# Kernel tuning notes

Measured on AMD Instinct MI355X. Metric: run time of the kernel, lower is better.

## Reference

```python
import jax, jax.numpy as jnp
import numpy as np
from jax import lax

D_MODEL = 512; D_FF = 2048
D_STATE = 16; D_CONV = 4; EXPAND = 2          # mamba_ssm defaults
D_INNER = EXPAND * D_MODEL                    # 1024
DT_RANK = (D_MODEL + 15) // 16                # 32
B, W, C, D = 2, 1024, 64, 8                   # C*D == D_MODEL


def setup_inputs():
    key = jax.random.key(0)
    ks = jax.random.split(key, 24)
    def p(k, shape, s=0.02):
        return jax.random.normal(k, shape, jnp.float32) * s
    inp = {"x": jax.random.normal(ks[0], (B, W, C, D), jnp.float32)}
    for i, pref in enumerate(["fm", "bm"]):
        o = 1 + i * 7
        inp[pref + "_in_W"] = p(ks[o], (2 * D_INNER, D_MODEL))
        inp[pref + "_conv_W"] = p(ks[o + 1], (D_INNER, D_CONV))
        inp[pref + "_conv_b"] = jnp.zeros((D_INNER,), jnp.float32)
        inp[pref + "_xproj_W"] = p(ks[o + 2], (DT_RANK + 2 * D_STATE, D_INNER))
        inp[pref + "_dt_W"] = p(ks[o + 3], (D_INNER, DT_RANK))
        inp[pref + "_dt_b"] = p(ks[o + 4], (D_INNER,), 0.1)
        inp[pref + "_A_log"] = jnp.log(jnp.broadcast_to(
            jnp.arange(1, D_STATE + 1, dtype=jnp.float32), (D_INNER, D_STATE)))
        inp[pref + "_D"] = jnp.ones((D_INNER,), jnp.float32)
        inp[pref + "_out_W"] = p(ks[o + 5], (D_MODEL, D_INNER))
    inp["ln1_g"] = jnp.ones((D_MODEL,), jnp.float32); inp["ln1_b"] = jnp.zeros((D_MODEL,), jnp.float32)
    inp["ln2_g"] = jnp.ones((D_MODEL,), jnp.float32); inp["ln2_b"] = jnp.zeros((D_MODEL,), jnp.float32)
    inp["ln3_g"] = jnp.ones((D_MODEL,), jnp.float32); inp["ln3_b"] = jnp.zeros((D_MODEL,), jnp.float32)
    inp["ff_W1"] = p(ks[15], (D_FF, D_MODEL)); inp["ff_b1"] = jnp.zeros((D_FF,), jnp.float32)
    inp["ff_W2"] = p(ks[16], (D_MODEL, D_FF)); inp["ff_b2"] = jnp.zeros((D_MODEL,), jnp.float32)
    return inp


def _silu(x):
    return x * jax.nn.sigmoid(x)


def _layernorm(x, g, b, eps=1e-5):
    mu = jnp.mean(x, -1, keepdims=True)
    var = jnp.var(x, -1, keepdims=True)
    return (x - mu) * lax.rsqrt(var + eps) * g + b


def _mamba(u, in_W, conv_W, conv_b, xproj_W, dt_W, dt_b, A_log, Dp, out_W):
    # u: (B, L, d_model). Standard Mamba block (mamba_ssm reference math).
    xz = jnp.einsum('bld,ed->ble', u, in_W)            # (B, L, 2*d_inner)
    xm, z = jnp.split(xz, 2, axis=-1)
    # causal depthwise conv along L
    xc = lax.conv_general_dilated(
        xm.transpose(0, 2, 1), conv_W[:, None, :], (1,),
        [(D_CONV - 1, 0)], feature_group_count=D_INNER)
    xm = _silu((xc + conv_b[None, :, None]).transpose(0, 2, 1))  # (B, L, d_inner)
    dbc = jnp.einsum('bld,ed->ble', xm, xproj_W)       # (B, L, dt_rank + 2*d_state)
    dt = dbc[..., :DT_RANK]
    Bm = dbc[..., DT_RANK:DT_RANK + D_STATE]           # (B, L, d_state)
    Cm = dbc[..., DT_RANK + D_STATE:]                  # (B, L, d_state)
    delta = jax.nn.softplus(jnp.einsum('blr,dr->bld', dt, dt_W) + dt_b)  # (B, L, d_inner)
    A = -jnp.exp(A_log)                                # (d_inner, d_state)
    dA = jnp.exp(delta[..., None] * A)                 # (B, L, d_inner, d_state)
    dBu = delta[..., None] * Bm[:, :, None, :] * xm[..., None]

    def step(h, inputs):
        dA_t, dBu_t = inputs
        h = dA_t * h + dBu_t
        return h, h

    h0 = jnp.zeros((u.shape[0], D_INNER, D_STATE), u.dtype)
    _, hs = lax.scan(step, h0, (dA.transpose(1, 0, 2, 3), dBu.transpose(1, 0, 2, 3)))
    y = jnp.einsum('lbds,lbs->bld', hs, Cm.transpose(1, 0, 2))
    y = y + xm * Dp
    y = y * _silu(z)
    return jnp.einsum('ble,de->bld', y, out_W)         # (B, L, d_model)


def reference(x,
              fm_in_W, fm_conv_W, fm_conv_b, fm_xproj_W, fm_dt_W, fm_dt_b, fm_A_log, fm_D, fm_out_W,
              bm_in_W, bm_conv_W, bm_conv_b, bm_xproj_W, bm_dt_W, bm_dt_b, bm_A_log, bm_D, bm_out_W,
              ln1_g, ln1_b, ln2_g, ln2_b, ln3_g, ln3_b,
              ff_W1, ff_b1, ff_W2, ff_b2):
    b, w, c, d = x.shape
    xf = x.reshape(b, w, c * d)
    fwd = _mamba(xf, fm_in_W, fm_conv_W, fm_conv_b, fm_xproj_W, fm_dt_W, fm_dt_b, fm_A_log, fm_D, fm_out_W)
    bwd = jnp.flip(_mamba(jnp.flip(xf, 1), bm_in_W, bm_conv_W, bm_conv_b, bm_xproj_W,
                          bm_dt_W, bm_dt_b, bm_A_log, bm_D, bm_out_W), 1)
    an1 = _layernorm(xf + fwd, ln1_g, ln1_b)   # AddNorm: LN(x + dropout(y)); dropout off at eval
    an2 = _layernorm(xf + bwd, ln2_g, ln2_b)
    out = an1 + an2
    h = jnp.maximum(jnp.einsum('bld,fd->blf', out, ff_W1) + ff_b1, 0)
    ff = jnp.einsum('blf,df->bld', h, ff_W2) + ff_b2
    out = _layernorm(ff + ff, ln3_g, ln3_b)    # an3(out, out) == LN(out + out)
    return out.reshape(b, w, c, d)
```

## Files before the change

kernel.cpp:

```cpp
#include <hip/hip_runtime.h>
#include <hip/hip_bf16.h>
#include <math.h>

#define MM 2048
#define BATCH 2
#define SEQ 1024
#define DMODEL 512
#define DINNER 1024
#define DSTATE 16
#define DTRANK 32
#define DFF 2048

#define NCHUNK 16
#define CHUNK 64
#define GTOT 65536

typedef short bf16x8 __attribute__((ext_vector_type(8)));
typedef float floatx4 __attribute__((ext_vector_type(4)));
typedef unsigned short ushort8v __attribute__((ext_vector_type(8)));
typedef unsigned short ushort4v __attribute__((ext_vector_type(4)));

__device__ __forceinline__ unsigned short f2bf(float f) {
    union { float f; unsigned u; } v; v.f = f;
    unsigned r = v.u + 0x7FFF + ((v.u >> 16) & 1);
    return (unsigned short)(r >> 16);
}
__device__ __forceinline__ float bf2f(unsigned short u) {
    union { unsigned u; float f; } v; v.u = ((unsigned)u) << 16; return v.f;
}

__device__ __forceinline__ float quadsum4(float x) {
    union { float f; int i; } a, b;
    a.f = x;
    b.i = __builtin_amdgcn_update_dpp(0, a.i, 0xB1, 0xF, 0xF, false); a.f += b.f;
    b.i = __builtin_amdgcn_update_dpp(0, a.i, 0x4E, 0xF, 0xF, false); a.f += b.f;
    return a.f;
}

#define GLOAD_LDS16(gp, lp) __builtin_amdgcn_global_load_lds( \
    (const __attribute__((address_space(1))) unsigned int*)(gp), \
    (__attribute__((address_space(3))) unsigned int*)(lp), 16, 0, 0)


template<int EPI, int OUTBF16>
__global__ __launch_bounds__(256) void gemm_mfma_batch(
    int M, int N, int K,
    const unsigned short* __restrict__ A0, const unsigned short* __restrict__ A1, int lda,
    const unsigned short* __restrict__ B0, const unsigned short* __restrict__ B1, int ldb,
    const float* __restrict__ bias,
    void* __restrict__ C0, void* __restrict__ C1, int ldc)
{
    __shared__ unsigned short As[2][128 * 32];
    __shared__ unsigned short Bs[2][128 * 32];
    const int z = blockIdx.z;
    const unsigned short* A = z ? A1 : A0;
    const unsigned short* B = z ? B1 : B0;
    void* Cout = z ? C1 : C0;
    const int tid  = threadIdx.x;
    const int wave = tid >> 6;
    const int lane = tid & 63;
    const int bm = blockIdx.y * 128;
    const int bn = blockIdx.x * 128;

    const int strow = lane & 15;
    const int stkc  = lane >> 4;
    const int wr = wave >> 1, wc = wave & 1;
    const int frow = lane & 15;
    const int fkc  = lane >> 4;

    floatx4 acc[4][4];
    #pragma unroll
    for (int i = 0; i < 4; ++i)
        #pragma unroll
        for (int j = 0; j < 4; ++j)
            acc[i][j] = (floatx4){0.f, 0.f, 0.f, 0.f};

    for (int k0 = 0; k0 < K; k0 += 64) {
        __syncthreads();
        #pragma unroll
        for (int hh = 0; hh < 2; ++hh) {
            #pragma unroll
            for (int q = 0; q < 2; ++q) {
                int g = wave * 2 + q;
                GLOAD_LDS16(A + (size_t)(bm + g * 16 + strow) * lda + k0 + hh * 32 + stkc * 8,
                            As[hh] + g * 512);
            }
            #pragma unroll
            for (int q = 0; q < 2; ++q) {
                int g = wave * 2 + q;
                GLOAD_LDS16(B + (size_t)(bn + g * 16 + strow) * ldb + k0 + hh * 32 + stkc * 8,
                            Bs[hh] + g * 512);
            }
        }
        __syncthreads();

        #pragma unroll
        for (int hh = 0; hh < 2; ++hh) {
            bf16x8 af[4], bfr[4];
            #pragma unroll
            for (int i = 0; i < 4; ++i)
                af[i] = *(const bf16x8*)(As[hh] + (wr * 4 + i) * 512 + fkc * 128 + frow * 8);
            #pragma unroll
            for (int j = 0; j < 4; ++j)
                bfr[j] = *(const bf16x8*)(Bs[hh] + (wc * 4 + j) * 512 + fkc * 128 + frow * 8);
            #pragma unroll
            for (int i = 0; i < 4; ++i)
                #pragma unroll
                for (int j = 0; j < 4; ++j)
                    acc[i][j] = __builtin_amdgcn_mfma_f32_16x16x32_bf16(
                        af[i], bfr[j], acc[i][j], 0, 0, 0);
        }
    }

    const int orow0 = bm + wr * 64 + (lane >> 4) * 4;
    const int ocol0 = bn + wc * 64 + (lane & 15);
    #pragma unroll
    for (int j = 0; j < 4; ++j) {
        const int col = ocol0 + j * 16;
        const float bv = bias ? bias[col] : 0.f;
        #pragma unroll
        for (int i = 0; i < 4; ++i) {
            #pragma unroll
            for (int r = 0; r < 4; ++r) {
                int row = orow0 + i * 16 + r;
                float t = acc[i][j][r] + bv;
                if (EPI == 1) t = fmaxf(t, 0.f);
                if (OUTBF16)
                    ((unsigned short*)Cout)[(size_t)row * ldc + col] = f2bf(t);
                else
                    ((float*)Cout)[(size_t)row * ldc + col] = t;
            }
        }
    }
}

__global__ __launch_bounds__(256) void gemm_inproj_kernel(
    const unsigned short* __restrict__ A,
    const unsigned short* __restrict__ B0, const unsigned short* __restrict__ B1,
    unsigned short* __restrict__ Cx0, unsigned short* __restrict__ Cz0,
    unsigned short* __restrict__ Cx1, unsigned short* __restrict__ Cz1)
{
    __shared__ unsigned short As[2][128 * 32];
    __shared__ unsigned short Bs[2][128 * 32];
    const int z = blockIdx.z;
    const unsigned short* B = z ? B1 : B0;
    const int tid  = threadIdx.x;
    const int wave = tid >> 6;
    const int lane = tid & 63;
    const int bm = blockIdx.y * 128;
    const int bn = blockIdx.x * 128;

    const int strow = lane & 15;
    const int stkc  = lane >> 4;
    const int wr = wave >> 1, wc = wave & 1;
    const int frow = lane & 15;
    const int fkc  = lane >> 4;

    floatx4 acc[4][4];
    #pragma unroll
    for (int i = 0; i < 4; ++i)
        #pragma unroll
        for (int j = 0; j < 4; ++j)
            acc[i][j] = (floatx4){0.f, 0.f, 0.f, 0.f};

    for (int k0 = 0; k0 < DMODEL; k0 += 64) {
        __syncthreads();
        #pragma unroll
        for (int hh = 0; hh < 2; ++hh) {
            #pragma unroll
            for (int q = 0; q < 2; ++q) {
                int g = wave * 2 + q;
                GLOAD_LDS16(A + (size_t)(bm + g * 16 + strow) * DMODEL + k0 + hh * 32 + stkc * 8,
                            As[hh] + g * 512);
            }
            #pragma unroll
            for (int q = 0; q < 2; ++q) {
                int g = wave * 2 + q;
                GLOAD_LDS16(B + (size_t)(bn + g * 16 + strow) * DMODEL + k0 + hh * 32 + stkc * 8,
                            Bs[hh] + g * 512);
            }
        }
        __syncthreads();

        #pragma unroll
        for (int hh = 0; hh < 2; ++hh) {
            bf16x8 af[4], bfr[4];
            #pragma unroll
            for (int i = 0; i < 4; ++i)
                af[i] = *(const bf16x8*)(As[hh] + (wr * 4 + i) * 512 + fkc * 128 + frow * 8);
            #pragma unroll
            for (int j = 0; j < 4; ++j)
                bfr[j] = *(const bf16x8*)(Bs[hh] + (wc * 4 + j) * 512 + fkc * 128 + frow * 8);
            #pragma unroll
            for (int i = 0; i < 4; ++i)
                #pragma unroll
                for (int j = 0; j < 4; ++j)
                    acc[i][j] = __builtin_amdgcn_mfma_f32_16x16x32_bf16(
                        af[i], bfr[j], acc[i][j], 0, 0, 0);
        }
    }

    const int zh = bn >= DINNER;
    unsigned short* C = z ? (zh ? Cz1 : Cx1) : (zh ? Cz0 : Cx0);
    const int cb = zh ? DINNER : 0;
    const int orow0 = bm + wr * 64 + (lane >> 4) * 4;
    const int ocol0 = bn + wc * 64 + (lane & 15) - cb;
    #pragma unroll
    for (int j = 0; j < 4; ++j) {
        const int col = ocol0 + j * 16;
        #pragma unroll
        for (int i = 0; i < 4; ++i)
            #pragma unroll
            for (int r = 0; r < 4; ++r)
                C[(size_t)(orow0 + i * 16 + r) * DINNER + col] = f2bf(acc[i][j][r]);
    }
}

template<int NSPLIT>
__global__ __launch_bounds__(256) void gemm_mfma_splitk(
    int M, int N, int K,
    const unsigned short* __restrict__ A0, const unsigned short* __restrict__ A1, int lda,
    const unsigned short* __restrict__ B0, const unsigned short* __restrict__ B1, int ldb,
    float* __restrict__ part, int ldc)
{
    __shared__ unsigned short As[2][128 * 32];
    __shared__ unsigned short Bs[2][128 * 32];
    const int z = blockIdx.z;
    const int dir = z / NSPLIT, sp = z % NSPLIT;
    const unsigned short* A = dir ? A1 : A0;
    const unsigned short* B = dir ? B1 : B0;
    float* Cp = part + (size_t)z * M * ldc;
    const int kbeg = sp * (K / NSPLIT);
    const int kend = kbeg + (K / NSPLIT);
    const int tid  = threadIdx.x;
    const int wave = tid >> 6;
    const int lane = tid & 63;
    const int bm = blockIdx.y * 128;
    const int bn = blockIdx.x * 128;

    const int strow = lane & 15;
    const int stkc  = lane >> 4;
    const int wr = wave >> 1, wc = wave & 1;
    const int frow = lane & 15;
    const int fkc  = lane >> 4;

    floatx4 acc[4][4];
    #pragma unroll
    for (int i = 0; i < 4; ++i)
        #pragma unroll
        for (int j = 0; j < 4; ++j)
            acc[i][j] = (floatx4){0.f, 0.f, 0.f, 0.f};

    for (int k0 = kbeg; k0 < kend; k0 += 64) {
        __syncthreads();
        #pragma unroll
        for (int hh = 0; hh < 2; ++hh) {
            #pragma unroll
            for (int q = 0; q < 2; ++q) {
                int g = wave * 2 + q;
                GLOAD_LDS16(A + (size_t)(bm + g * 16 + strow) * lda + k0 + hh * 32 + stkc * 8,
                            As[hh] + g * 512);
            }
            #pragma unroll
            for (int q = 0; q < 2; ++q) {
                int g = wave * 2 + q;
                GLOAD_LDS16(B + (size_t)(bn + g * 16 + strow) * ldb + k0 + hh * 32 + stkc * 8,
                            Bs[hh] + g * 512);
            }
        }
        __syncthreads();

        #pragma unroll
        for (int hh = 0; hh < 2; ++hh) {
            bf16x8 af[4], bfr[4];
            #pragma unroll
            for (int i = 0; i < 4; ++i)
                af[i] = *(const bf16x8*)(As[hh] + (wr * 4 + i) * 512 + fkc * 128 + frow * 8);
            #pragma unroll
            for (int j = 0; j < 4; ++j)
                bfr[j] = *(const bf16x8*)(Bs[hh] + (wc * 4 + j) * 512 + fkc * 128 + frow * 8);
            #pragma unroll
            for (int i = 0; i < 4; ++i)
                #pragma unroll
                for (int j = 0; j < 4; ++j)
                    acc[i][j] = __builtin_amdgcn_mfma_f32_16x16x32_bf16(
                        af[i], bfr[j], acc[i][j], 0, 0, 0);
        }
    }

    const int orow0 = bm + wr * 64 + (lane >> 4) * 4;
    const int ocol0 = bn + wc * 64 + (lane & 15);
    #pragma unroll
    for (int j = 0; j < 4; ++j) {
        const int col = ocol0 + j * 16;
        #pragma unroll
        for (int i = 0; i < 4; ++i)
            #pragma unroll
            for (int r = 0; r < 4; ++r)
                Cp[(size_t)(orow0 + i * 16 + r) * ldc + col] = acc[i][j][r];
    }
}

__global__ __launch_bounds__(256) void xproj_splitk_kernel(
    const unsigned short* __restrict__ A_f, const unsigned short* __restrict__ A_b,
    const unsigned short* __restrict__ Wf,  const unsigned short* __restrict__ Wb,
    float* __restrict__ part)
{
    __shared__ unsigned short As[2][128 * 32];
    __shared__ unsigned short Bs[2][64 * 32];
    const int tid = threadIdx.x, wave = tid >> 6, lane = tid & 63;
    const int bm = blockIdx.x * 128;
    const int dir = blockIdx.y >> 2, sp = blockIdx.y & 3;
    const unsigned short* A = dir ? A_b : A_f;
    const unsigned short* W = dir ? Wb  : Wf;
    float* Cp = part + (size_t)blockIdx.y * MM * 64;
    const int kbeg = sp * 256, kend = kbeg + 256;

    const int strow = lane & 15;
    const int stkc  = lane >> 4;
    const int frow = lane & 15;
    const int fkc  = lane >> 4;

    floatx4 acc[2][4];
    #pragma unroll
    for (int i = 0; i < 2; ++i)
        #pragma unroll
        for (int j = 0; j < 4; ++j)
            acc[i][j] = (floatx4){0.f, 0.f, 0.f, 0.f};

    for (int k0 = kbeg; k0 < kend; k0 += 64) {
        __syncthreads();
        #pragma unroll
        for (int hh = 0; hh < 2; ++hh) {
            #pragma unroll
            for (int q = 0; q < 2; ++q) {
                int g = wave * 2 + q;
                GLOAD_LDS16(A + (size_t)(bm + g * 16 + strow) * DINNER + k0 + hh * 32 + stkc * 8,
                            As[hh] + g * 512);
            }
            GLOAD_LDS16(W + (size_t)(wave * 16 + strow) * DINNER + k0 + hh * 32 + stkc * 8,
                        Bs[hh] + wave * 512);
        }
        __syncthreads();

        #pragma unroll
        for (int hh = 0; hh < 2; ++hh) {
            bf16x8 af[2], bfr[4];
            #pragma unroll
            for (int i = 0; i < 2; ++i)
                af[i] = *(const bf16x8*)(As[hh] + (wave * 2 + i) * 512 + fkc * 128 + frow * 8);
            #pragma unroll
            for (int j = 0; j < 4; ++j)
                bfr[j] = *(const bf16x8*)(Bs[hh] + j * 512 + fkc * 128 + frow * 8);
            #pragma unroll
            for (int i = 0; i < 2; ++i)
                #pragma unroll
                for (int j = 0; j < 4; ++j)
                    acc[i][j] = __builtin_amdgcn_mfma_f32_16x16x32_bf16(
                        af[i], bfr[j], acc[i][j], 0, 0, 0);
        }
    }

    const int orow0 = bm + wave * 32 + (lane >> 4) * 4;
    #pragma unroll
    for (int j = 0; j < 4; ++j) {
        const int col = (lane & 15) + j * 16;
        #pragma unroll
        for (int i = 0; i < 2; ++i)
            #pragma unroll
            for (int r = 0; r < 4; ++r)
                Cp[(size_t)(orow0 + i * 16 + r) * 64 + col] = acc[i][j][r];
    }
}

__global__ __launch_bounds__(256) void xproj_reduce_kernel(
    const float* __restrict__ part,
    float* __restrict__ dbc_f, float* __restrict__ dbc_b,
    float* __restrict__ bct_f, float* __restrict__ bct_b)
{
    const int dir = blockIdx.y;
    const int i = (blockIdx.x * 256 + threadIdx.x) * 4;
    const float* p = part + (size_t)dir * 4 * (MM * 64);
    float4 a = *(const float4*)(p + i);
    #pragma unroll
    for (int s = 1; s < 4; ++s) {
        float4 t = *(const float4*)(p + (size_t)s * (MM * 64) + i);
        a.x += t.x; a.y += t.y; a.z += t.z; a.w += t.w;
    }
    const int m = i >> 6, c = i & 63;
    if (c < 32) {
        float* dbc = dir ? dbc_b : dbc_f;
        *(float4*)(dbc + (size_t)m * 32 + c) = a;
    } else {
        float* bct = dir ? bct_b : bct_f;
        *(float4*)(bct + (size_t)m * 32 + (c - 32)) = a;
    }
}

__global__ __launch_bounds__(256) void dtproj_batch_kernel(
    int M, int N, int K,
    const float* __restrict__ A0, const float* __restrict__ A1, int lda,
    const float* __restrict__ B0, const float* __restrict__ B1, int ldb,
    const float* __restrict__ bias0, const float* __restrict__ bias1,
    unsigned short* __restrict__ C0, unsigned short* __restrict__ C1, int ldc)
{
    __shared__ float As[16][64];
    __shared__ float Bs[16][64];
    const int z = blockIdx.z;
    const float* A = z ? A1 : A0;
    const float* B = z ? B1 : B0;
    const float* biasR = z ? bias1 : bias0;
    unsigned short* C = z ? C1 : C0;
    const int tid = threadIdx.x;
    const int tx = tid & 15, ty = tid >> 4;
    const int bm = blockIdx.y * 64, bn = blockIdx.x * 64;
    const int lm = tid & 63;
    const int lk = (tid >> 6) * 4;
    const float* Arow = A + (size_t)(bm + lm) * lda + lk;
    const float* Brow = B + (size_t)(bn + lm) * ldb + lk;
    float acc[4][4] = {};
    for (int k0 = 0; k0 < K; k0 += 16) {
        float4 av = *(const float4*)(Arow + k0);
        float4 bv = *(const float4*)(Brow + k0);
        __syncthreads();
        As[lk+0][lm] = av.x; As[lk+1][lm] = av.y; As[lk+2][lm] = av.z; As[lk+3][lm] = av.w;
        Bs[lk+0][lm] = bv.x; Bs[lk+1][lm] = bv.y; Bs[lk+2][lm] = bv.z; Bs[lk+3][lm] = bv.w;
        __syncthreads();
        #pragma unroll
        for (int k = 0; k < 16; ++k) {
            float4 a = *(const float4*)(&As[k][ty*4]);
            float4 b = *(const float4*)(&Bs[k][tx*4]);
            float ar[4] = {a.x,a.y,a.z,a.w};
            float br[4] = {b.x,b.y,b.z,b.w};
            #pragma unroll
            for (int i = 0; i < 4; ++i)
                #pragma unroll
                for (int j = 0; j < 4; ++j)
                    acc[i][j] = fmaf(ar[i], br[j], acc[i][j]);
        }
    }
    const int row0 = bm + ty*4, col0 = bn + tx*4;
    #pragma unroll
    for (int i = 0; i < 4; ++i) {
        float br = biasR[row0 + i];
        ushort4v o;
        #pragma unroll
        for (int j = 0; j < 4; ++j) {
            float t = acc[i][j] + br;
            o[j] = f2bf(fmaxf(t, 0.f) + log1pf(__expf(-fabsf(t))));
        }
        *(ushort4v*)(C + (size_t)(row0 + i) * ldc + col0) = o;
    }
}

__global__ __launch_bounds__(256) void cast_pre_kernel(
    const float* __restrict__ x, const float* __restrict__ w0,
    const float* __restrict__ w1, const float* __restrict__ xp0,
    const float* __restrict__ xp1, unsigned short* __restrict__ dst)
{
    int i = (blockIdx.x * 256 + threadIdx.x) * 8;
    const float* src; int off;
    if      (i < 1048576) { src = x;   off = 0; }
    else if (i < 2097152) { src = w0;  off = 1048576; }
    else if (i < 3145728) { src = w1;  off = 2097152; }
    else if (i < 3211264) { src = xp0; off = 3145728; }
    else                  { src = xp1; off = 3211264; }
    float4 a = *(const float4*)(src + i - off);
    float4 b = *(const float4*)(src + i - off + 4);
    ushort8v o;
    o[0] = f2bf(a.x); o[1] = f2bf(a.y); o[2] = f2bf(a.z); o[3] = f2bf(a.w);
    o[4] = f2bf(b.x); o[5] = f2bf(b.y); o[6] = f2bf(b.z); o[7] = f2bf(b.w);
    *(ushort8v*)(dst + i) = o;
}

__global__ __launch_bounds__(256) void cast_post_kernel(
    const float* __restrict__ w0, const float* __restrict__ w1,
    const float* __restrict__ w2, const float* __restrict__ w3,
    unsigned short* __restrict__ dst)
{
    int i = (blockIdx.x * 256 + threadIdx.x) * 8;
    const float* src; int off;
    if      (i < 524288)  { src = w0; off = 0; }
    else if (i < 1048576) { src = w1; off = 524288; }
    else if (i < 2097152) { src = w2; off = 1048576; }
    else                  { src = w3; off = 2097152; }
    float4 a = *(const float4*)(src + i - off);
    float4 b = *(const float4*)(src + i - off + 4);
    ushort8v o;
    o[0] = f2bf(a.x); o[1] = f2bf(a.y); o[2] = f2bf(a.z); o[3] = f2bf(a.w);
    o[4] = f2bf(b.x); o[5] = f2bf(b.y); o[6] = f2bf(b.z); o[7] = f2bf(b.w);
    *(ushort8v*)(dst + i) = o;
}

__global__ __launch_bounds__(256) void conv_silu_tr_kernel(
    const unsigned short* __restrict__ x_f, const unsigned short* __restrict__ x_b,
    const float* __restrict__ Wf,  const float* __restrict__ Wb,
    const float* __restrict__ cbf, const float* __restrict__ cbb,
    unsigned short* __restrict__ of,  unsigned short* __restrict__ ob,
    unsigned short* __restrict__ otf, unsigned short* __restrict__ otb)
{
    __shared__ unsigned short t[32][34];
    const int dir = blockIdx.z;
    const unsigned short* xo = dir ? x_b : x_f;
    const float* convW = dir ? Wb : Wf;
    const float* convb = dir ? cbb : cbf;
    unsigned short* xm  = dir ? ob : of;
    unsigned short* xmT = dir ? otb : otf;
    const int m0 = blockIdx.x * 32, d0 = blockIdx.y * 32;
    const int tx = threadIdx.x & 31, ty = threadIdx.x >> 5;
    const int d = d0 + tx;
    float4 wv = *(const float4*)(convW + d * 4);
    float w[4] = {wv.x, wv.y, wv.z, wv.w};
    const float cb = convb[d];
    #pragma unroll
    for (int rr = 0; rr < 32; rr += 8) {
        int m = m0 + ty + rr;
        int b = m >> 10, l = m & (SEQ - 1);
        float acc = cb;
        #pragma unroll
        for (int j = 0; j < 4; ++j) {
            int p = dir ? (l + 3 - j) : (l - 3 + j);
            if (p >= 0 && p < SEQ)
                acc = fmaf(bf2f(xo[(size_t)(b * SEQ + p) * DINNER + d]), w[j], acc);
        }
        float sig = 1.f / (1.f + __expf(-acc));
        unsigned short v = f2bf(acc * sig);
        xm[(size_t)m * DINNER + d] = v;
        t[ty + rr][tx] = v;
    }
    __syncthreads();
    #pragma unroll
    for (int rr = 0; rr < 32; rr += 8)
        xmT[(size_t)(d0 + ty + rr) * MM + m0 + tx] = t[tx][ty + rr];
}

template<int DIR>
__device__ __forceinline__ void pass1_body(
    const unsigned short* __restrict__ deltaT, const unsigned short* __restrict__ xmT,
    const float* __restrict__ bct, const float* __restrict__ Alog,
    const float* __restrict__ Dv,
    unsigned short* __restrict__ y0T, float* __restrict__ cumT,
    float* __restrict__ Pout, float* __restrict__ Hout)
{
    const int tid = threadIdx.x;
    const int sq = tid & 3;
    const int dloc = tid >> 2;
    const int d = blockIdx.x * 64 + dloc;
    const int b = blockIdx.y / NCHUNK;
    const int c = blockIdx.y % NCHUNK;

    float4 Av = *(const float4*)(Alog + d * DSTATE + sq * 4);
    const float A0 = -__expf(Av.x), A1 = -__expf(Av.y);
    const float A2 = -__expf(Av.z), A3 = -__expf(Av.w);
    const float Dp = Dv[d];
    const unsigned short* dRow = deltaT + (size_t)d * MM + b * SEQ;
    const unsigned short* xRow = xmT + (size_t)d * MM + b * SEQ;
    const float* bcRow = bct + (size_t)(b * SEQ) * 32 + sq * 4;
    unsigned short* yRow = y0T + (size_t)d * MM + b * SEQ;
    float* uRow = cumT + (size_t)d * MM + b * SEQ;

    float h0 = 0.f, h1 = 0.f, h2 = 0.f, h3 = 0.f, sdl = 0.f;
    const int segBase = DIR ? (SEQ - CHUNK - c * CHUNK) : (c * CHUNK);
    for (int ii = 0; ii < CHUNK; ii += 8) {
        const int off = DIR ? (segBase + (CHUNK - 8) - ii) : (segBase + ii);
        ushort8v dl8 = *(const ushort8v*)(dRow + off);
        ushort8v x8  = *(const ushort8v*)(xRow + off);
        float yv[8], cu[8];
        #pragma unroll
        for (int u = 0; u < 8; ++u) {
            const int t = DIR ? (7 - u) : u;
            float4 Bv = *(const float4*)(bcRow + (size_t)(off + t) * 32);
            float4 Cv = *(const float4*)(bcRow + (size_t)(off + t) * 32 + 16);
            float dlv = bf2f(dl8[t]);
            float xv  = bf2f(x8[t]);
            sdl += dlv;
            float dx = dlv * xv;
            h0 = fmaf(__expf(dlv * A0), h0, dx * Bv.x);
            h1 = fmaf(__expf(dlv * A1), h1, dx * Bv.y);
            h2 = fmaf(__expf(dlv * A2), h2, dx * Bv.z);
            h3 = fmaf(__expf(dlv * A3), h3, dx * Bv.w);
            float part = h0 * Cv.x + h1 * Cv.y + h2 * Cv.z + h3 * Cv.w;
            part = quadsum4(part);
            yv[t] = fmaf(xv, Dp, part);
            cu[t] = sdl;
        }
        if (sq == 0) {
            ushort8v y8;
            #pragma unroll
            for (int u = 0; u < 8; ++u) y8[u] = f2bf(yv[u]);
            *(ushort8v*)(yRow + off) = y8;
            *(float4*)(uRow + off)     = (float4){cu[0], cu[1], cu[2], cu[3]};
            *(float4*)(uRow + off + 4) = (float4){cu[4], cu[5], cu[6], cu[7]};
        }
    }
    const size_t g4 = ((size_t)(DIR * BATCH + b) * DINNER + d) * DSTATE + sq * 4;
    *(float4*)(Pout + (size_t)c * GTOT + g4) =
        (float4){__expf(sdl * A0), __expf(sdl * A1), __expf(sdl * A2), __expf(sdl * A3)};
    *(float4*)(Hout + (size_t)c * GTOT + g4) = (float4){h0, h1, h2, h3};
}

__global__ __launch_bounds__(256) void scan_pass1_kernel(
    const unsigned short* __restrict__ dT_f, const unsigned short* __restrict__ dT_b,
    const unsigned short* __restrict__ xT_f, const unsigned short* __restrict__ xT_b,
    const float* __restrict__ bct_f, const float* __restrict__ bct_b,
    const float* __restrict__ Alog_f, const float* __restrict__ Alog_b,
    const float* __restrict__ D_f, const float* __restrict__ D_b,
    unsigned short* __restrict__ y0T_f, unsigned short* __restrict__ y0T_b,
    float* __restrict__ cumT_f, float* __restrict__ cumT_b,
    float* __restrict__ Pout, float* __restrict__ Hout)
{
    if (blockIdx.z == 0)
        pass1_body<0>(dT_f, xT_f, bct_f, Alog_f, D_f, y0T_f, cumT_f, Pout, Hout);
    else
        pass1_body<1>(dT_b, xT_b, bct_b, Alog_b, D_b, y0T_b, cumT_b, Pout, Hout);
}

__global__ __launch_bounds__(256) void scan_carry_kernel(
    const float* __restrict__ P, const float* __restrict__ H,
    float* __restrict__ carry)
{
    const int g = blockIdx.x * 256 + threadIdx.x;
    float p[NCHUNK], hh[NCHUNK];
    #pragma unroll
    for (int c = 0; c < NCHUNK; ++c) {
        p[c]  = P[(size_t)c * GTOT + g];
        hh[c] = H[(size_t)c * GTOT + g];
    }
    float h = 0.f;
    #pragma unroll
    for (int c = 0; c < NCHUNK; ++c) {
        carry[(size_t)c * GTOT + g] = h;
        h = fmaf(p[c], h, hh[c]);
    }
}

__global__ __launch_bounds__(256) void scan_correct_kernel(
    const unsigned short* __restrict__ y0T_f, const unsigned short* __restrict__ y0T_b,
    const float* __restrict__ cumT_f, const float* __restrict__ cumT_b,
    const float* __restrict__ bct_f, const float* __restrict__ bct_b,
    const float* __restrict__ Alog_f, const float* __restrict__ Alog_b,
    const float* __restrict__ carry,
    const unsigned short* __restrict__ z_f, const unsigned short* __restrict__ z_b,
    unsigned short* __restrict__ ybf_f, unsigned short* __restrict__ ybf_b)
{
    __shared__ float Cs[16][33];
    __shared__ float Asm[32][16];
    __shared__ float Cy[32][16];
    __shared__ float t[32][33];

    const int dir = blockIdx.z;
    const unsigned short* y0T = dir ? y0T_b : y0T_f;
    const float* cumT = dir ? cumT_b : cumT_f;
    const float* bct  = dir ? bct_b  : bct_f;
    const float* Alog = dir ? Alog_b : Alog_f;
    const unsigned short* zon = dir ? z_b : z_f;
    unsigned short* ybf = dir ? ybf_b : ybf_f;

    const int m0 = blockIdx.x * 32, d0 = blockIdx.y * 32;
    const int b = m0 >> 10;
    const int l0 = m0 & (SEQ - 1);
    const int c = dir ? ((SEQ - 1 - l0) >> 6) : (l0 >> 6);

    for (int idx = threadIdx.x; idx < 512; idx += 256) {
        int s1 = idx & 15, ml = idx >> 4;
        Cs[s1][ml] = bct[(size_t)(m0 + ml) * 32 + 16 + s1];
        int dl2 = idx >> 4, s2 = idx & 15;
        Asm[dl2][s2] = -__expf(Alog[(d0 + dl2) * DSTATE + s2]);
        Cy[dl2][s2] = carry[(size_t)c * GTOT
            + ((size_t)(dir * BATCH + b) * DINNER + d0 + dl2) * DSTATE + s2];
    }
    __syncthreads();

    const int tx = threadIdx.x & 31, ty = threadIdx.x >> 5;
    #pragma unroll
    for (int rr = 0; rr < 32; rr += 8) {
        const int dloc = ty + rr;
        const size_t base = (size_t)(d0 + dloc) * MM + m0 + tx;
        float u  = cumT[base];
        float y0 = bf2f(y0T[base]);
        float corr = 0.f;
        #pragma unroll
        for (int s = 0; s < DSTATE; ++s)
            corr = fmaf(Cs[s][tx] * Cy[dloc][s], __expf(Asm[dloc][s] * u), corr);
        t[dloc][tx] = y0 + corr;
    }
    __syncthreads();
    #pragma unroll
    for (int rr = 0; rr < 32; rr += 8) {
        int m = m0 + ty + rr, d = d0 + tx;
        float z = bf2f(zon[(size_t)m * DINNER + d]);
        float sig = 1.f / (1.f + __expf(-z));
        ybf[(size_t)m * DINNER + d] = f2bf(t[tx][ty + rr] * (z * sig));
    }
}

__global__ __launch_bounds__(256) void reduce_ff1_kernel(
    const float* __restrict__ part, const float* __restrict__ bias,
    unsigned short* __restrict__ outh)
{
    const int i = (blockIdx.x * 256 + threadIdx.x) * 4;
    float4 a = *(const float4*)(part + i);
    float4 b = *(const float4*)(part + (size_t)MM * DFF + i);
    const int c = i & (DFF - 1);
    ushort4v o;
    o[0] = f2bf(fmaxf(a.x + b.x + bias[c],     0.f));
    o[1] = f2bf(fmaxf(a.y + b.y + bias[c + 1], 0.f));
    o[2] = f2bf(fmaxf(a.z + b.z + bias[c + 2], 0.f));
    o[3] = f2bf(fmaxf(a.w + b.w + bias[c + 3], 0.f));
    *(ushort4v*)(outh + i) = o;
}

__global__ __launch_bounds__(256) void ln_combine_fused_kernel(
    const float* __restrict__ xf, const float* __restrict__ part,
    const float* __restrict__ g1, const float* __restrict__ b1,
    const float* __restrict__ g2, const float* __restrict__ b2,
    unsigned short* __restrict__ out)
{
    const int m = blockIdx.x;
    const int tid = threadIdx.x;
    const size_t stride = (size_t)MM * DMODEL;
    const float* xr = xf + (size_t)m * DMODEL;
    const float* p = part + (size_t)m * DMODEL;
    float v1a = xr[tid], v1b = xr[tid + 256];
    float v2a = xr[tid], v2b = xr[tid + 256];
    #pragma unroll
    for (int k = 0; k < 4; ++k) {
        v1a += p[k * stride + tid];       v1b += p[k * stride + tid + 256];
        v2a += p[(4 + k) * stride + tid]; v2b += p[(4 + k) * stride + tid + 256];
    }
    float s1 = v1a + v1b, q1 = v1a*v1a + v1b*v1b;
    float s2 = v2a + v2b, q2 = v2a*v2a + v2b*v2b;
    #pragma unroll
    for (int off = 32; off; off >>= 1) {
        s1 += __shfl_xor(s1, off); q1 += __shfl_xor(q1, off);
        s2 += __shfl_xor(s2, off); q2 += __shfl_xor(q2, off);
    }
    __shared__ float sm[4][4];
    const int w = tid >> 6;
    if ((tid & 63) == 0) { sm[w][0] = s1; sm[w][1] = q1; sm[w][2] = s2; sm[w][3] = q2; }
    __syncthreads();
    s1 = sm[0][0] + sm[1][0] + sm[2][0] + sm[3][0];
    q1 = sm[0][1] + sm[1][1] + sm[2][1] + sm[3][1];
    s2 = sm[0][2] + sm[1][2] + sm[2][2] + sm[3][2];
    q2 = sm[0][3] + sm[1][3] + sm[2][3] + sm[3][3];
    const float inv = 1.f / DMODEL;
    float mu1 = s1 * inv, mu2 = s2 * inv;
    float rs1 = rsqrtf(q1 * inv - mu1 * mu1 + 1e-5f);
    float rs2 = rsqrtf(q2 * inv - mu2 * mu2 + 1e-5f);
    unsigned short* orow = out + (size_t)m * DMODEL;
    orow[tid]       = f2bf((v1a - mu1) * rs1 * g1[tid]       + b1[tid]
                         + (v2a - mu2) * rs2 * g2[tid]       + b2[tid]);
    orow[tid + 256] = f2bf((v1b - mu1) * rs1 * g1[tid + 256] + b1[tid + 256]
                         + (v2b - mu2) * rs2 * g2[tid + 256] + b2[tid + 256]);
}

__global__ __launch_bounds__(256) void ln_final_fused_kernel(
    const float* __restrict__ part, const float* __restrict__ bias,
    const float* __restrict__ g, const float* __restrict__ b,
    float* __restrict__ out)
{
    const int m = blockIdx.x;
    const int tid = threadIdx.x;
    const size_t stride = (size_t)MM * DMODEL;
    const float* p = part + (size_t)m * DMODEL;
    float fa = bias[tid], fb = bias[tid + 256];
    #pragma unroll
    for (int k = 0; k < 8; ++k) {
        fa += p[k * stride + tid];
        fb += p[k * stride + tid + 256];
    }
    float va = 2.f * fa, vb = 2.f * fb;
    float s = va + vb, q = va*va + vb*vb;
    #pragma unroll
    for (int off = 32; off; off >>= 1) {
        s += __shfl_xor(s, off); q += __shfl_xor(q, off);
    }
    __shared__ float sm[4][2];
    const int w = tid >> 6;
    if ((tid & 63) == 0) { sm[w][0] = s; sm[w][1] = q; }
    __syncthreads();
    s = sm[0][0] + sm[1][0] + sm[2][0] + sm[3][0];
    q = sm[0][1] + sm[1][1] + sm[2][1] + sm[3][1];
    const float inv = 1.f / DMODEL;
    float mu = s * inv;
    float rs = rsqrtf(q * inv - mu * mu + 1e-5f);
    float* orow = out + (size_t)m * DMODEL;
    orow[tid]       = (va - mu) * rs * g[tid]       + b[tid];
    orow[tid + 256] = (vb - mu) * rs * g[tid + 256] + b[tid + 256];
}

extern "C" void kernel_launch(void* const* d_in, const int* in_sizes, int n_in,
                              void* d_out, int out_size, void* d_ws, size_t ws_size,
                              hipStream_t stream)
{
    const float* x         = (const float*)d_in[0];
    const float* fm_in_W   = (const float*)d_in[1];
    const float* fm_conv_W = (const float*)d_in[2];
    const float* fm_conv_b = (const float*)d_in[3];
    const float* fm_xproj_W= (const float*)d_in[4];
    const float* fm_dt_W   = (const float*)d_in[5];
    const float* fm_dt_b   = (const float*)d_in[6];
    const float* fm_A_log  = (const float*)d_in[7];
    const float* fm_D      = (const float*)d_in[8];
    const float* fm_out_W  = (const float*)d_in[9];
    const float* bm_in_W   = (const float*)d_in[10];
    const float* bm_conv_W = (const float*)d_in[11];
    const float* bm_conv_b = (const float*)d_in[12];
    const float* bm_xproj_W= (const float*)d_in[13];
    const float* bm_dt_W   = (const float*)d_in[14];
    const float* bm_dt_b   = (const float*)d_in[15];
    const float* bm_A_log  = (const float*)d_in[16];
    const float* bm_D      = (const float*)d_in[17];
    const float* bm_out_W  = (const float*)d_in[18];
    const float* ln1_g     = (const float*)d_in[19];
    const float* ln1_b     = (const float*)d_in[20];
    const float* ln2_g     = (const float*)d_in[21];
    const float* ln2_b     = (const float*)d_in[22];
    const float* ln3_g     = (const float*)d_in[23];
    const float* ln3_b     = (const float*)d_in[24];
    const float* ff_W1     = (const float*)d_in[25];
    const float* ff_b1     = (const float*)d_in[26];
    const float* ff_W2     = (const float*)d_in[27];
    const float* ff_b2     = (const float*)d_in[28];
    float* out = (float*)d_out;

    float* ws = (float*)d_ws;
    size_t o = 0;
    unsigned short* xbf_f = (unsigned short*)(ws + o); o += (size_t)MM * DINNER / 2;
    unsigned short* xbf_b = (unsigned short*)(ws + o); o += (size_t)MM * DINNER / 2;
    unsigned short* zbf_f = (unsigned short*)(ws + o); o += (size_t)MM * DINNER / 2;
    unsigned short* zbf_b = (unsigned short*)(ws + o); o += (size_t)MM * DINNER / 2;
    unsigned short* xm_bf_f = (unsigned short*)(ws + o); o += (size_t)MM * DINNER / 2;
    unsigned short* xm_bf_b = (unsigned short*)(ws + o); o += (size_t)MM * DINNER / 2;
    unsigned short* xmT_f   = (unsigned short*)(ws + o); o += (size_t)MM * DINNER / 2;
    unsigned short* xmT_b   = (unsigned short*)(ws + o); o += (size_t)MM * DINNER / 2;
    unsigned short* deltaT_f= (unsigned short*)(ws + o); o += (size_t)MM * DINNER / 2;
    unsigned short* deltaT_b= (unsigned short*)(ws + o); o += (size_t)MM * DINNER / 2;
    float* dbc_f    = ws + o; o += (size_t)MM * 32;
    float* dbc_b    = ws + o; o += (size_t)MM * 32;
    float* bct_f    = ws + o; o += (size_t)MM * 32;
    float* bct_b    = ws + o; o += (size_t)MM * 32;
    unsigned short* y0T_f = (unsigned short*)(ws + o); o += (size_t)MM * DINNER / 2;
    unsigned short* y0T_b = (unsigned short*)(ws + o); o += (size_t)MM * DINNER / 2;
    float* scanP    = ws + o; o += (size_t)NCHUNK * (GTOT / 16) * 16;
    float* scanH    = ws + o; o += (size_t)NCHUNK * (GTOT / 16) * 16;
    float* scanCy   = ws + o; o += (size_t)NCHUNK * (GTOT / 16) * 16;
    float* gpart    = ws + o; o += (size_t)8 * MM * DMODEL;

    float* cumT_f = gpart;
    float* cumT_b = gpart + (size_t)MM * DINNER;
    unsigned short* xin_bf     = (unsigned short*)scanP;
    unsigned short* fm_inW_bf  = xin_bf + 1048576;
    unsigned short* bm_inW_bf  = fm_inW_bf + 1048576;
    unsigned short* fm_xpW_bf  = bm_inW_bf + 1048576;
    unsigned short* bm_xpW_bf  = fm_xpW_bf + 65536;
    unsigned short* ybf_f = (unsigned short*)scanP;
    unsigned short* ybf_b = (unsigned short*)scanH;
    unsigned short* fm_outW_bf = (unsigned short*)zbf_f;
    unsigned short* bm_outW_bf = fm_outW_bf + 524288;
    unsigned short* W1_bf      = bm_outW_bf + 524288;
    unsigned short* W2_bf      = W1_bf + 1048576;
    unsigned short* outsum_bf  = (unsigned short*)xbf_f;
    unsigned short* h_bf = (unsigned short*)deltaT_f;

    cast_pre_kernel<<<3276800 / 2048, 256, 0, stream>>>(
        x, fm_in_W, bm_in_W, fm_xproj_W, bm_xproj_W, xin_bf);

    gemm_inproj_kernel<<<dim3(2048/128, MM/128, 2), 256, 0, stream>>>(
        xin_bf, fm_inW_bf, bm_inW_bf, xbf_f, zbf_f, xbf_b, zbf_b);

    conv_silu_tr_kernel<<<dim3(MM/32, DINNER/32, 2), 256, 0, stream>>>(
        xbf_f, xbf_b, fm_conv_W, bm_conv_W, fm_conv_b, bm_conv_b,
        xm_bf_f, xm_bf_b, xmT_f, xmT_b);

    xproj_splitk_kernel<<<dim3(MM/128, 8), 256, 0, stream>>>(
        xm_bf_f, xm_bf_b, fm_xpW_bf, bm_xpW_bf, gpart);
    xproj_reduce_kernel<<<dim3((MM*64)/1024, 2), 256, 0, stream>>>(
        gpart, dbc_f, dbc_b, bct_f, bct_b);

    dtproj_batch_kernel<<<dim3(MM/64, DINNER/64, 2), 256, 0, stream>>>(
        DINNER, MM, DTRANK, fm_dt_W, bm_dt_W, DTRANK, dbc_f, dbc_b, 32,
        fm_dt_b, bm_dt_b, deltaT_f, deltaT_b, MM);

    scan_pass1_kernel<<<dim3(DINNER/64, BATCH*NCHUNK, 2), 256, 0, stream>>>(
        deltaT_f, deltaT_b, xmT_f, xmT_b, bct_f, bct_b,
        fm_A_log, bm_A_log, fm_D, bm_D,
        y0T_f, y0T_b, cumT_f, cumT_b, scanP, scanH);
    scan_carry_kernel<<<GTOT/256, 256, 0, stream>>>(scanP, scanH, scanCy);
    scan_correct_kernel<<<dim3(MM/32, DINNER/32, 2), 256, 0, stream>>>(
        y0T_f, y0T_b, cumT_f, cumT_b, bct_f, bct_b, fm_A_log, bm_A_log,
        scanCy, zbf_f, zbf_b, ybf_f, ybf_b);

    cast_post_kernel<<<3145728 / 2048, 256, 0, stream>>>(
        fm_out_W, bm_out_W, ff_W1, ff_W2, fm_outW_bf);

    gemm_mfma_splitk<4><<<dim3(DMODEL/128, MM/128, 8), 256, 0, stream>>>(
        MM, DMODEL, DINNER, ybf_f, ybf_b, DINNER, fm_outW_bf, bm_outW_bf, DINNER,
        gpart, DMODEL);

    ln_combine_fused_kernel<<<MM, 256, 0, stream>>>(
        x, gpart, ln1_g, ln1_b, ln2_g, ln2_b, outsum_bf);

    gemm_mfma_splitk<2><<<dim3(DFF/128, MM/128, 2), 256, 0, stream>>>(
        MM, DFF, DMODEL, outsum_bf, outsum_bf, DMODEL, W1_bf, W1_bf, DMODEL,
        gpart, DFF);
    reduce_ff1_kernel<<<(MM*DFF)/1024, 256, 0, stream>>>(gpart, ff_b1, h_bf);

    gemm_mfma_splitk<8><<<dim3(DMODEL/128, MM/128, 8), 256, 0, stream>>>(
        MM, DMODEL, DFF, h_bf, h_bf, DFF, W2_bf, W2_bf, DFF, gpart, DMODEL);

    ln_final_fused_kernel<<<MM, 256, 0, stream>>>(
        gpart, ff_b2, ln3_g, ln3_b, out);
}
```

Measured before the change: 308.1 us.

## Halve split-K partials and fuse FF1 bias+ReLU into a non-split GEMM

Reduces split-K depth for the out-projection and FF2 GEMMs from 8 to 4 slices, so the fused LayerNorm kernels read half as many fp32 partial buffers. The FF1 GEMM switches from split-K plus a separate reduce kernel to a single batch GEMM with bias+ReLU and a bf16 epilogue, which removes one launch and an fp32 round-trip through memory. The trade-off is fewer workgroups per GEMM, so latency hiding and CU occupancy may be lower on the large GPU. It assumes gemm_mfma_batch<1,1> supports this bias/ReLU epilogue signature.

```diff
diff --git a/kernel.cpp b/kernel.cpp
--- a/kernel.cpp
+++ b/kernel.cpp
@@ -694,22 +694,6 @@
     }
 }
 
-__global__ __launch_bounds__(256) void reduce_ff1_kernel(
-    const float* __restrict__ part, const float* __restrict__ bias,
-    unsigned short* __restrict__ outh)
-{
-    const int i = (blockIdx.x * 256 + threadIdx.x) * 4;
-    float4 a = *(const float4*)(part + i);
-    float4 b = *(const float4*)(part + (size_t)MM * DFF + i);
-    const int c = i & (DFF - 1);
-    ushort4v o;
-    o[0] = f2bf(fmaxf(a.x + b.x + bias[c],     0.f));
-    o[1] = f2bf(fmaxf(a.y + b.y + bias[c + 1], 0.f));
-    o[2] = f2bf(fmaxf(a.z + b.z + bias[c + 2], 0.f));
-    o[3] = f2bf(fmaxf(a.w + b.w + bias[c + 3], 0.f));
-    *(ushort4v*)(outh + i) = o;
-}
-
 __global__ __launch_bounds__(256) void ln_combine_fused_kernel(
     const float* __restrict__ xf, const float* __restrict__ part,
     const float* __restrict__ g1, const float* __restrict__ b1,
@@ -721,13 +705,10 @@
     const size_t stride = (size_t)MM * DMODEL;
     const float* xr = xf + (size_t)m * DMODEL;
     const float* p = part + (size_t)m * DMODEL;
-    float v1a = xr[tid], v1b = xr[tid + 256];
-    float v2a = xr[tid], v2b = xr[tid + 256];
-    #pragma unroll
-    for (int k = 0; k < 4; ++k) {
-        v1a += p[k * stride + tid];       v1b += p[k * stride + tid + 256];
-        v2a += p[(4 + k) * stride + tid]; v2b += p[(4 + k) * stride + tid + 256];
-    }
+    float v1a = xr[tid]       + p[tid]              + p[stride + tid];
+    float v1b = xr[tid + 256] + p[tid + 256]        + p[stride + tid + 256];
+    float v2a = xr[tid]       + p[2*stride + tid]   + p[3*stride + tid];
+    float v2b = xr[tid + 256] + p[2*stride + tid + 256] + p[3*stride + tid + 256];
     float s1 = v1a + v1b, q1 = v1a*v1a + v1b*v1b;
     float s2 = v2a + v2b, q2 = v2a*v2a + v2b*v2b;
     #pragma unroll
@@ -763,12 +744,10 @@
     const int tid = threadIdx.x;
     const size_t stride = (size_t)MM * DMODEL;
     const float* p = part + (size_t)m * DMODEL;
-    float fa = bias[tid], fb = bias[tid + 256];
-    #pragma unroll
-    for (int k = 0; k < 8; ++k) {
-        fa += p[k * stride + tid];
-        fb += p[k * stride + tid + 256];
-    }
+    float fa = bias[tid]       + p[tid]       + p[stride + tid]
+             + p[2*stride + tid]       + p[3*stride + tid];
+    float fb = bias[tid + 256] + p[tid + 256] + p[stride + tid + 256]
+             + p[2*stride + tid + 256] + p[3*stride + tid + 256];
     float va = 2.f * fa, vb = 2.f * fb;
     float s = va + vb, q = va*va + vb*vb;
     #pragma unroll
@@ -845,7 +824,7 @@
     float* scanP    = ws + o; o += (size_t)NCHUNK * (GTOT / 16) * 16;
     float* scanH    = ws + o; o += (size_t)NCHUNK * (GTOT / 16) * 16;
     float* scanCy   = ws + o; o += (size_t)NCHUNK * (GTOT / 16) * 16;
-    float* gpart    = ws + o; o += (size_t)8 * MM * DMODEL;
+    float* gpart    = ws + o; o += (size_t)4 * MM * DMODEL;
 
     float* cumT_f = gpart;
     float* cumT_b = gpart + (size_t)MM * DINNER;
@@ -894,19 +873,18 @@
     cast_post_kernel<<<3145728 / 2048, 256, 0, stream>>>(
         fm_out_W, bm_out_W, ff_W1, ff_W2, fm_outW_bf);
 
-    gemm_mfma_splitk<4><<<dim3(DMODEL/128, MM/128, 8), 256, 0, stream>>>(
+    gemm_mfma_splitk<2><<<dim3(DMODEL/128, MM/128, 4), 256, 0, stream>>>(
         MM, DMODEL, DINNER, ybf_f, ybf_b, DINNER, fm_outW_bf, bm_outW_bf, DINNER,
         gpart, DMODEL);
 
     ln_combine_fused_kernel<<<MM, 256, 0, stream>>>(
         x, gpart, ln1_g, ln1_b, ln2_g, ln2_b, outsum_bf);
 
-    gemm_mfma_splitk<2><<<dim3(DFF/128, MM/128, 2), 256, 0, stream>>>(
+    gemm_mfma_batch<1,1><<<dim3(DFF/128, MM/128, 1), 256, 0, stream>>>(
         MM, DFF, DMODEL, outsum_bf, outsum_bf, DMODEL, W1_bf, W1_bf, DMODEL,
-        gpart, DFF);
-    reduce_ff1_kernel<<<(MM*DFF)/1024, 256, 0, stream>>>(gpart, ff_b1, h_bf);
-
-    gemm_mfma_splitk<8><<<dim3(DMODEL/128, MM/128, 8), 256, 0, stream>>>(
+        ff_b1, h_bf, h_bf, DFF);
+
+    gemm_mfma_splitk<4><<<dim3(DMODEL/128, MM/128, 4), 256, 0, stream>>>(
         MM, DMODEL, DFF, h_bf, h_bf, DFF, W2_bf, W2_bf, DFF, gpart, DMODEL);
 
     ln_final_fused_kernel<<<MM, 256, 0, stream>>>(
```

Measured after the change: 301.7 us. -2.1%, faster.
